# Performance work log

Hardware: AMD Instinct MI355X
Metric: run time of the kernel (lower is better)

The kernel has to match this reference:

```python
import jax, jax.numpy as jnp
import numpy as np

B, NPTS, NBASIS, DIM, H, CH = 8, 1024, 8, 8, 512, 16
EPSILON = 1000.0
P = 2
VOLUME = 2.0 ** DIM  # MC domain [-1,1]^dim


def setup_inputs() -> dict:
    key = jax.random.key(0)
    ks = jax.random.split(key, 10)
    s = jax.random.uniform(ks[0], (NPTS, DIM), dtype=jnp.float32) * 2.0 - 1.0  # MC samples in [-1,1]^dim
    x = jax.random.uniform(ks[1], (1, DIM), dtype=jnp.float32) * 2.0 - 1.0     # eval point
    Wfirst = jax.random.normal(ks[2], (DIM, H), dtype=jnp.float32) / np.sqrt(DIM)
    bfirst = jax.random.normal(ks[3], (H,), dtype=jnp.float32) * 0.01
    Wb = jax.random.normal(ks[4], (NBASIS, H, H), dtype=jnp.float32) / np.sqrt(H)
    bb = jax.random.normal(ks[5], (NBASIS, H), dtype=jnp.float32) * 0.01
    Wlast = jax.random.normal(ks[6], (H, CH), dtype=jnp.float32) / np.sqrt(H)
    blast = jax.random.normal(ks[7], (CH,), dtype=jnp.float32) * 0.01
    Wf = jax.random.normal(ks[8], (DIM, CH), dtype=jnp.float32) / np.sqrt(DIM)
    bf = jax.random.normal(ks[9], (CH,), dtype=jnp.float32) * 0.01
    return dict(s=s, x=x, Wfirst=Wfirst, bfirst=bfirst, Wb=Wb, bb=bb,
                Wlast=Wlast, blast=blast, Wf=Wf, bf=bf)


def _basis_all(pts, Wfirst, bfirst, Wb, bb, Wlast, blast):
    # pts: [M, DIM] -> all n basis nets, batch-repeated: [NBASIS, B, M, CH]
    a0 = jax.nn.elu(jnp.einsum('md,dh->mh', pts, Wfirst) + bfirst)          # [M, H]
    a0 = jnp.broadcast_to(a0[None], (B,) + a0.shape)                         # [B, M, H] (repeat over batch)
    a1 = jax.nn.elu(jnp.einsum('bmh,ihk->ibmk', a0, Wb) + bb[:, None, None, :])  # [n, B, M, H]
    return jnp.einsum('ibmk,kc->ibmc', a1, Wlast) + blast                    # [n, B, M, CH]


def reference(s, x, Wfirst, bfirst, Wb, bb, Wlast, blast, Wf, bf):
    # func(s): linear map realizing the projected function  [NPTS, CH]
    f_s = jnp.einsum('nd,dc->nc', s, Wf) + bf
    basis_s = _basis_all(s, Wfirst, bfirst, Wb, bb, Wlast, blast)            # [n, B, NPTS, CH]
    diff = f_s[None, None] - basis_s                                          # broadcast over n, B
    # Monte Carlo integral of (func - basis_i)^p over [-1,1]^dim, per channel
    integral = VOLUME * jnp.mean(diff ** P, axis=-2)                          # [n, B, CH]
    norm_pc = integral ** (1.0 / P)                                           # Lp norm per channel
    norm_b = jnp.sum(jnp.abs(norm_pc) ** P, axis=-1, keepdims=True) ** (1.0 / P)  # [n, B, 1]
    mu = jnp.where(norm_b <= EPSILON, norm_b, 0.0)                            # [n, B, 1]
    basis_x = _basis_all(x, Wfirst, bfirst, Wb, bb, Wlast, blast)[:, :, 0, :]  # [n, B, CH]
    out = jnp.sum(mu * basis_x, axis=0)                                       # [B, CH]
    normalization = 1e-7 + jnp.sum(mu, axis=0)                                # [B, 1]
    return out / normalization
```

## Files before the change

kernel.cpp:

```cpp
#include <hip/hip_runtime.h>

typedef _Float16 half8 __attribute__((ext_vector_type(8)));
typedef float f32x4 __attribute__((ext_vector_type(4)));
typedef float f32x16 __attribute__((ext_vector_type(16)));
typedef unsigned int u32x4 __attribute__((ext_vector_type(4)));

#define NPTS 1024
#define NB 8
#define HDIM 512
#define CH 16
#define RT 1056

#define OFF_WBH 0u
#define OFF_WBL (4u*1024u*1024u)
#define OFF_A0H (8u*1024u*1024u)
#define A0SZ    (64u*RT*8u*2u)
#define OFF_A0L (OFF_A0H + A0SZ)
#define OFF_WLH (OFF_A0L + A0SZ)
#define OFF_WLL (OFF_WLH + 16384u)
#define OFF_FS  (OFF_WLL + 16384u)
#define OFF_PP  (OFF_FS + 65536u)
#define PPSZ    (8u*2u*RT*16u*4u)
#define OFF_IP  (OFF_PP + PPSZ)
#define OFF_BX  (OFF_IP + 2048u)

__device__ __forceinline__ float elu(float z) { return z > 0.f ? z : expm1f(z); }

__global__ __launch_bounds__(256) void kPrep(const float* __restrict__ s,
    const float* __restrict__ x, const float* __restrict__ Wfirst,
    const float* __restrict__ bfirst, const float* __restrict__ Wb,
    const float* __restrict__ Wlast, const float* __restrict__ Wf,
    const float* __restrict__ bf,
    _Float16* __restrict__ Wbh, _Float16* __restrict__ Wbl,
    _Float16* __restrict__ WlH, _Float16* __restrict__ WlL,
    _Float16* __restrict__ a0h, _Float16* __restrict__ a0l,
    float* __restrict__ f_s) {
  __shared__ __align__(16) float sm[8192];
  int b = blockIdx.x, t = threadIdx.x;
  if (b < 512) {
    int i = b >> 6, koct = b & 63;
    int j = t >> 5, c = t & 31;
    const float* src = Wb + ((size_t)i * 512 + koct * 8 + j) * 512;
#pragma unroll
    for (int e = 0; e < 4; ++e)
      *(f32x4*)&sm[j * 512 + (e * 32 + c) * 4] = *(const f32x4*)&src[(e * 32 + c) * 4];
    __syncthreads();
#pragma unroll
    for (int p = 0; p < 2; ++p) {
      int n = t + p * 256;
      union { _Float16 h[8]; u32x4 u; } hu, lu;
#pragma unroll
      for (int jj = 0; jj < 8; ++jj) {
        float v = sm[jj * 512 + n];
        _Float16 hv = (_Float16)v;
        hu.h[jj] = hv;
        lu.h[jj] = (_Float16)(v - (float)hv);
      }
      size_t o = ((size_t)(i * 64 + koct) * 512 + n) * 8;
      *(u32x4*)(Wbh + o) = hu.u;
      *(u32x4*)(Wbl + o) = lu.u;
    }
  } else if (b < 776) {
    int rr = t >> 6, tl = t & 63;
    int m = (b - 512) * 4 + rr;
    float* sv = &sm[rr * 8];
    if (tl < 8) sv[tl] = (m < 1024) ? s[m * 8 + tl] : (m == 1024 ? x[tl] : 0.f);
    __syncthreads();
    size_t o = ((size_t)tl * RT + m) * 8;
    if (m <= 1024) {
      float acc[8];
#pragma unroll
      for (int jj = 0; jj < 8; ++jj) acc[jj] = bfirst[8 * tl + jj];
#pragma unroll
      for (int d = 0; d < 8; ++d) {
        float sd = sv[d];
        f32x4 w0 = *(const f32x4*)&Wfirst[d * 512 + 8 * tl];
        f32x4 w1 = *(const f32x4*)&Wfirst[d * 512 + 8 * tl + 4];
#pragma unroll
        for (int e = 0; e < 4; ++e) { acc[e] += sd * w0[e]; acc[4 + e] += sd * w1[e]; }
      }
      union { _Float16 h[8]; u32x4 u; } hu, lu;
#pragma unroll
      for (int jj = 0; jj < 8; ++jj) {
        float v = elu(acc[jj]);
        _Float16 hv = (_Float16)v;
        hu.h[jj] = hv;
        lu.h[jj] = (_Float16)(v - (float)hv);
      }
      *(u32x4*)(a0h + o) = hu.u;
      *(u32x4*)(a0l + o) = lu.u;
      if (m < 1024 && tl < 16) {
        float a = bf[tl];
#pragma unroll
        for (int d = 0; d < 8; ++d) a += sv[d] * Wf[d * 16 + tl];
        f_s[m * 16 + tl] = a;
      }
    } else {
      u32x4 z;
#pragma unroll
      for (int e = 0; e < 4; ++e) z[e] = 0u;
      *(u32x4*)(a0h + o) = z;
      *(u32x4*)(a0l + o) = z;
    }
  } else {
#pragma unroll
    for (int it = 0; it < 32; ++it) sm[t + 256 * it] = Wlast[t + 256 * it];
    __syncthreads();
#pragma unroll
    for (int p = 0; p < 4; ++p) {
      int oi = p * 256 + t;
      int ko = oi >> 4, ch = oi & 15;
      union { _Float16 h[8]; u32x4 u; } hu, lu;
#pragma unroll
      for (int jj = 0; jj < 8; ++jj) {
        float v = sm[(ko * 8 + jj) * 16 + ch];
        _Float16 hv = (_Float16)v;
        hu.h[jj] = hv;
        lu.h[jj] = (_Float16)(v - (float)hv);
      }
      *(u32x4*)(WlH + oi * 8) = hu.u;
      *(u32x4*)(WlL + oi * 8) = lu.u;
    }
  }
}

__global__ __launch_bounds__(256, 2) void kB(const _Float16* __restrict__ Wbh,
    const _Float16* __restrict__ Wbl, const _Float16* __restrict__ a0h,
    const _Float16* __restrict__ a0l, const _Float16* __restrict__ WlH,
    const _Float16* __restrict__ WlL, const float* __restrict__ bb,
    float* __restrict__ Pp) {
  __shared__ u32x4 AH[2048];
  __shared__ u32x4 AL[2048];
  __shared__ float S2[32][16];
  int t = threadIdx.x, b = blockIdx.x;
  int i = b & 7, r2 = b >> 3;
  int nh = r2 & 1, mt = r2 >> 1;
  int m0 = mt * 32, nb0 = nh * 256;
  int w = t >> 6, lane = t & 63, ln = lane & 31, q = lane >> 5, q4 = lane >> 4;

  const u32x4* a0h4 = (const u32x4*)a0h;
  const u32x4* a0l4 = (const u32x4*)a0l;
#pragma unroll
  for (int it = 0; it < 8; ++it) {
    int o = t + 256 * it;
    size_t g = (size_t)(o >> 5) * RT + m0 + (o & 31);
    AH[o] = a0h4[g];
    AL[o] = a0l4[g];
  }
  __syncthreads();

  int nwb = nb0 + w * 64;
  const u32x4* bh4 = (const u32x4*)Wbh;
  const u32x4* bl4 = (const u32x4*)Wbl;
  f32x16 hh0, hh1, hl0, hl1, lh0, lh1;
#pragma unroll
  for (int r = 0; r < 16; ++r) { hh0[r]=0.f; hh1[r]=0.f; hl0[r]=0.f; hl1[r]=0.f; lh0[r]=0.f; lh1[r]=0.f; }

#pragma unroll 4
  for (int ks = 0; ks < 32; ++ks) {
    int koct = ks * 2 + q;
    half8 aH = __builtin_bit_cast(half8, AH[koct * 32 + ln]);
    half8 aL = __builtin_bit_cast(half8, AL[koct * 32 + ln]);
    size_t bo = ((size_t)(i * 64 + koct)) * 512 + nwb + ln;
    half8 bH0 = __builtin_bit_cast(half8, bh4[bo]);
    half8 bH1 = __builtin_bit_cast(half8, bh4[bo + 32]);
    half8 bL0 = __builtin_bit_cast(half8, bl4[bo]);
    half8 bL1 = __builtin_bit_cast(half8, bl4[bo + 32]);
    hh0 = __builtin_amdgcn_mfma_f32_32x32x16_f16(aH, bH0, hh0, 0, 0, 0);
    hh1 = __builtin_amdgcn_mfma_f32_32x32x16_f16(aH, bH1, hh1, 0, 0, 0);
    hl0 = __builtin_amdgcn_mfma_f32_32x32x16_f16(aH, bL0, hl0, 0, 0, 0);
    hl1 = __builtin_amdgcn_mfma_f32_32x32x16_f16(aH, bL1, hl1, 0, 0, 0);
    lh0 = __builtin_amdgcn_mfma_f32_32x32x16_f16(aL, bH0, lh0, 0, 0, 0);
    lh1 = __builtin_amdgcn_mfma_f32_32x32x16_f16(aL, bH1, lh1, 0, 0, 0);
  }

  float zv[2][16];
#pragma unroll
  for (int r = 0; r < 16; ++r) {
    zv[0][r] = hh0[r] + hl0[r] + lh0[r];
    zv[1][r] = hh1[r] + hl1[r] + lh1[r];
  }
  __syncthreads();
  for (int o = t; o < 512; o += 256) ((float*)S2)[o] = 0.f;

  _Float16* scrH = (_Float16*)&AH[w * 512];
  _Float16* scrL = (_Float16*)&AH[w * 512 + 256];
#pragma unroll
  for (int nt = 0; nt < 2; ++nt)
#pragma unroll
    for (int r = 0; r < 16; ++r) {
      int row = (r & 3) + 8 * (r >> 2) + 4 * q;
      int kl = nt * 32 + ln;
      int h = nb0 + w * 64 + kl;
      float a1 = elu(zv[nt][r] + bb[i * 512 + h]);
      _Float16 hv = (_Float16)a1;
      _Float16 lv = (_Float16)(a1 - (float)hv);
      int oi = (row >> 4) * 128 + (kl >> 3) * 16 + (row & 15);
      scrH[oi * 8 + (kl & 7)] = hv;
      scrL[oi * 8 + (kl & 7)] = lv;
    }
  __syncthreads();

  int hb8 = (nb0 + w * 64) >> 3;
  const u32x4* wh4 = (const u32x4*)WlH;
  const u32x4* wl4 = (const u32x4*)WlL;
  const u32x4* sH4 = &AH[w * 512];
  const u32x4* sL4 = &AH[w * 512 + 256];
#pragma unroll
  for (int mt2 = 0; mt2 < 2; ++mt2) {
    f32x4 D2;
#pragma unroll
    for (int r = 0; r < 4; ++r) D2[r] = 0.f;
#pragma unroll
    for (int ks2 = 0; ks2 < 2; ++ks2) {
      int ai = mt2 * 128 + (ks2 * 4 + q4) * 16 + (lane & 15);
      half8 pH = __builtin_bit_cast(half8, sH4[ai]);
      half8 pL = __builtin_bit_cast(half8, sL4[ai]);
      size_t wo = (size_t)(hb8 + ks2 * 4 + q4) * 16 + (lane & 15);
      half8 wH = __builtin_bit_cast(half8, wh4[wo]);
      half8 wL = __builtin_bit_cast(half8, wl4[wo]);
      D2 = __builtin_amdgcn_mfma_f32_16x16x32_f16(pH, wH, D2, 0, 0, 0);
      D2 = __builtin_amdgcn_mfma_f32_16x16x32_f16(pH, wL, D2, 0, 0, 0);
      D2 = __builtin_amdgcn_mfma_f32_16x16x32_f16(pL, wH, D2, 0, 0, 0);
    }
#pragma unroll
    for (int r = 0; r < 4; ++r)
      atomicAdd(&S2[mt2 * 16 + q4 * 4 + r][lane & 15], D2[r]);
  }
  __syncthreads();
  for (int o = t; o < 512; o += 256) {
    int m = o >> 4, ch = o & 15;
    Pp[((size_t)(i * 2 + nh) * RT + m0 + m) * 16 + ch] = S2[m][ch];
  }
}

__global__ __launch_bounds__(256) void kTail(const float* __restrict__ Pp,
    const float* __restrict__ f_s, const float* __restrict__ blast,
    float* __restrict__ Ipart, float* __restrict__ basisx) {
  __shared__ float R[16][16];
  int b = blockIdx.x, t = threadIdx.x;
  if (b < 32) {
    int i = b >> 2, mq = b & 3;
    int ch = t & 15, g = t >> 4;
    float bl = blast[ch];
    const float* P0 = Pp + (size_t)(i * 2) * RT * 16;
    const float* P1 = Pp + (size_t)(i * 2 + 1) * RT * 16;
    float loc = 0.f;
#pragma unroll
    for (int it = 0; it < 16; ++it) {
      int m = mq * 256 + g + 16 * it;
      float bs = P0[m * 16 + ch] + P1[m * 16 + ch] + bl;
      float d = f_s[m * 16 + ch] - bs;
      loc += d * d;
    }
    R[g][ch] = loc;
    __syncthreads();
    if (t < 16) {
      float ssum = 0.f;
#pragma unroll
      for (int gg = 0; gg < 16; ++gg) ssum += R[gg][t];
      Ipart[(i * 4 + mq) * 16 + t] = ssum;
    }
  } else if (t < 128) {
    int i = t >> 4, ch = t & 15;
    basisx[t] = Pp[((size_t)(i * 2) * RT + 1024) * 16 + ch]
              + Pp[((size_t)(i * 2 + 1) * RT + 1024) * 16 + ch] + blast[ch];
  }
}

__global__ __launch_bounds__(128) void kFin(const float* __restrict__ Ipart,
    const float* __restrict__ basisx, float* __restrict__ out) {
  __shared__ float muL[8];
  int t = threadIdx.x;
  if (t < 8) {
    float S = 0.f;
#pragma unroll
    for (int qq = 0; qq < 64; ++qq) S += Ipart[t * 64 + qq];
    float nb = 0.5f * sqrtf(S);
    muL[t] = (nb <= 1000.0f) ? nb : 0.f;
  }
  __syncthreads();
  int ch = t & 15;
  float num = 0.f, den = 1e-7f;
#pragma unroll
  for (int i = 0; i < NB; ++i) {
    num += muL[i] * basisx[i * 16 + ch];
    den += muL[i];
  }
  out[t] = num / den;
}

extern "C" void kernel_launch(void* const* d_in, const int* in_sizes, int n_in,
                              void* d_out, int out_size, void* d_ws, size_t ws_size,
                              hipStream_t stream) {
  const float* s      = (const float*)d_in[0];
  const float* x      = (const float*)d_in[1];
  const float* Wfirst = (const float*)d_in[2];
  const float* bfirst = (const float*)d_in[3];
  const float* Wb     = (const float*)d_in[4];
  const float* bb     = (const float*)d_in[5];
  const float* Wlast  = (const float*)d_in[6];
  const float* blast  = (const float*)d_in[7];
  const float* Wf     = (const float*)d_in[8];
  const float* bf     = (const float*)d_in[9];

  char* ws = (char*)d_ws;
  _Float16* Wbh = (_Float16*)(ws + OFF_WBH);
  _Float16* Wbl = (_Float16*)(ws + OFF_WBL);
  _Float16* a0h = (_Float16*)(ws + OFF_A0H);
  _Float16* a0l = (_Float16*)(ws + OFF_A0L);
  _Float16* WlH = (_Float16*)(ws + OFF_WLH);
  _Float16* WlL = (_Float16*)(ws + OFF_WLL);
  float* f_s    = (float*)(ws + OFF_FS);
  float* Pp     = (float*)(ws + OFF_PP);
  float* Ipart  = (float*)(ws + OFF_IP);
  float* basisx = (float*)(ws + OFF_BX);
  float* out    = (float*)d_out;

  kPrep<<<777, 256, 0, stream>>>(s, x, Wfirst, bfirst, Wb, Wlast, Wf, bf,
                                 Wbh, Wbl, WlH, WlL, a0h, a0l, f_s);
  kB<<<528, 256, 0, stream>>>(Wbh, Wbl, a0h, a0l, WlH, WlL, bb, Pp);
  kTail<<<33, 256, 0, stream>>>(Pp, f_s, blast, Ipart, basisx);
  kFin<<<1, 128, 0, stream>>>(Ipart, basisx, out);
}
```

Baseline: 128.6 us.

## Split kB over four N-quarters with register double-buffered global loads

The main GEMM kernel now gives each block a quarter of the hidden dimension (32 columns per wave) instead of half. It drops the LDS staging of a0 and streams A and B fragments straight from global memory into a register double buffer, so the block count doubles and occupancy can rise to three blocks per CU. Weight conversion in kPrep drops its LDS transpose and uses more blocks with strided direct loads. kTail now reduces each basis in a single block and computes mu directly, leaving kFin with less work. The cost is reading a0 from global once per N-quarter with no LDS reuse, and more partial sums in Pp that the tail must read.

```diff
diff --git a/kernel.cpp b/kernel.cpp
--- a/kernel.cpp
+++ b/kernel.cpp
@@ -20,9 +20,9 @@
 #define OFF_WLL (OFF_WLH + 16384u)
 #define OFF_FS  (OFF_WLL + 16384u)
 #define OFF_PP  (OFF_FS + 65536u)
-#define PPSZ    (8u*2u*RT*16u*4u)
-#define OFF_IP  (OFF_PP + PPSZ)
-#define OFF_BX  (OFF_IP + 2048u)
+#define PPSZ    (8u*4u*RT*16u*4u)
+#define OFF_MU  (OFF_PP + PPSZ)
+#define OFF_BX  (OFF_MU + 64u)
 
 __device__ __forceinline__ float elu(float z) { return z > 0.f ? z : expm1f(z); }
 
@@ -37,32 +37,25 @@
     float* __restrict__ f_s) {
   __shared__ __align__(16) float sm[8192];
   int b = blockIdx.x, t = threadIdx.x;
-  if (b < 512) {
-    int i = b >> 6, koct = b & 63;
-    int j = t >> 5, c = t & 31;
-    const float* src = Wb + ((size_t)i * 512 + koct * 8 + j) * 512;
-#pragma unroll
-    for (int e = 0; e < 4; ++e)
-      *(f32x4*)&sm[j * 512 + (e * 32 + c) * 4] = *(const f32x4*)&src[(e * 32 + c) * 4];
-    __syncthreads();
-#pragma unroll
-    for (int p = 0; p < 2; ++p) {
-      int n = t + p * 256;
-      union { _Float16 h[8]; u32x4 u; } hu, lu;
-#pragma unroll
-      for (int jj = 0; jj < 8; ++jj) {
-        float v = sm[jj * 512 + n];
-        _Float16 hv = (_Float16)v;
-        hu.h[jj] = hv;
-        lu.h[jj] = (_Float16)(v - (float)hv);
-      }
-      size_t o = ((size_t)(i * 64 + koct) * 512 + n) * 8;
-      *(u32x4*)(Wbh + o) = hu.u;
-      *(u32x4*)(Wbl + o) = lu.u;
-    }
-  } else if (b < 776) {
+  if (b < 1024) {
+    int i = b >> 7, koct = (b >> 1) & 63, n = (b & 1) * 256 + t;
+    const float* src = Wb + ((size_t)i * 512 + koct * 8) * 512 + n;
+    float v[8];
+#pragma unroll
+    for (int j = 0; j < 8; ++j) v[j] = src[j * 512];
+    union { _Float16 h[8]; u32x4 u; } hu, lu;
+#pragma unroll
+    for (int j = 0; j < 8; ++j) {
+      _Float16 hv = (_Float16)v[j];
+      hu.h[j] = hv;
+      lu.h[j] = (_Float16)(v[j] - (float)hv);
+    }
+    size_t o = ((size_t)(i * 64 + koct) * 512 + n) * 8;
+    *(u32x4*)(Wbh + o) = hu.u;
+    *(u32x4*)(Wbl + o) = lu.u;
+  } else if (b < 1288) {
     int rr = t >> 6, tl = t & 63;
-    int m = (b - 512) * 4 + rr;
+    int m = (b - 1024) * 4 + rr;
     float* sv = &sm[rr * 8];
     if (tl < 8) sv[tl] = (m < 1024) ? s[m * 8 + tl] : (m == 1024 ? x[tl] : 0.f);
     __syncthreads();
@@ -124,161 +117,153 @@
   }
 }
 
-__global__ __launch_bounds__(256, 2) void kB(const _Float16* __restrict__ Wbh,
+__global__ __launch_bounds__(256, 3) void kB(const _Float16* __restrict__ Wbh,
     const _Float16* __restrict__ Wbl, const _Float16* __restrict__ a0h,
     const _Float16* __restrict__ a0l, const _Float16* __restrict__ WlH,
     const _Float16* __restrict__ WlL, const float* __restrict__ bb,
     float* __restrict__ Pp) {
-  __shared__ u32x4 AH[2048];
-  __shared__ u32x4 AL[2048];
+  __shared__ u32x4 SC[1024];
   __shared__ float S2[32][16];
   int t = threadIdx.x, b = blockIdx.x;
-  int i = b & 7, r2 = b >> 3;
-  int nh = r2 & 1, mt = r2 >> 1;
-  int m0 = mt * 32, nb0 = nh * 256;
+  int i = b & 7, r = b >> 3;
+  int nq = r & 3, mt = r >> 2;
+  int m0 = mt * 32;
   int w = t >> 6, lane = t & 63, ln = lane & 31, q = lane >> 5, q4 = lane >> 4;
+  int nw = nq * 128 + w * 32;
 
   const u32x4* a0h4 = (const u32x4*)a0h;
   const u32x4* a0l4 = (const u32x4*)a0l;
-#pragma unroll
-  for (int it = 0; it < 8; ++it) {
-    int o = t + 256 * it;
-    size_t g = (size_t)(o >> 5) * RT + m0 + (o & 31);
-    AH[o] = a0h4[g];
-    AL[o] = a0l4[g];
-  }
-  __syncthreads();
-
-  int nwb = nb0 + w * 64;
-  const u32x4* bh4 = (const u32x4*)Wbh;
-  const u32x4* bl4 = (const u32x4*)Wbl;
-  f32x16 hh0, hh1, hl0, hl1, lh0, lh1;
-#pragma unroll
-  for (int r = 0; r < 16; ++r) { hh0[r]=0.f; hh1[r]=0.f; hl0[r]=0.f; hl1[r]=0.f; lh0[r]=0.f; lh1[r]=0.f; }
-
-#pragma unroll 4
-  for (int ks = 0; ks < 32; ++ks) {
-    int koct = ks * 2 + q;
-    half8 aH = __builtin_bit_cast(half8, AH[koct * 32 + ln]);
-    half8 aL = __builtin_bit_cast(half8, AL[koct * 32 + ln]);
-    size_t bo = ((size_t)(i * 64 + koct)) * 512 + nwb + ln;
-    half8 bH0 = __builtin_bit_cast(half8, bh4[bo]);
-    half8 bH1 = __builtin_bit_cast(half8, bh4[bo + 32]);
-    half8 bL0 = __builtin_bit_cast(half8, bl4[bo]);
-    half8 bL1 = __builtin_bit_cast(half8, bl4[bo + 32]);
-    hh0 = __builtin_amdgcn_mfma_f32_32x32x16_f16(aH, bH0, hh0, 0, 0, 0);
-    hh1 = __builtin_amdgcn_mfma_f32_32x32x16_f16(aH, bH1, hh1, 0, 0, 0);
-    hl0 = __builtin_amdgcn_mfma_f32_32x32x16_f16(aH, bL0, hl0, 0, 0, 0);
-    hl1 = __builtin_amdgcn_mfma_f32_32x32x16_f16(aH, bL1, hl1, 0, 0, 0);
-    lh0 = __builtin_amdgcn_mfma_f32_32x32x16_f16(aL, bH0, lh0, 0, 0, 0);
-    lh1 = __builtin_amdgcn_mfma_f32_32x32x16_f16(aL, bH1, lh1, 0, 0, 0);
-  }
-
-  float zv[2][16];
-#pragma unroll
-  for (int r = 0; r < 16; ++r) {
-    zv[0][r] = hh0[r] + hl0[r] + lh0[r];
-    zv[1][r] = hh1[r] + hl1[r] + lh1[r];
-  }
-  __syncthreads();
-  for (int o = t; o < 512; o += 256) ((float*)S2)[o] = 0.f;
-
-  _Float16* scrH = (_Float16*)&AH[w * 512];
-  _Float16* scrL = (_Float16*)&AH[w * 512 + 256];
-#pragma unroll
-  for (int nt = 0; nt < 2; ++nt)
-#pragma unroll
-    for (int r = 0; r < 16; ++r) {
-      int row = (r & 3) + 8 * (r >> 2) + 4 * q;
-      int kl = nt * 32 + ln;
-      int h = nb0 + w * 64 + kl;
-      float a1 = elu(zv[nt][r] + bb[i * 512 + h]);
-      _Float16 hv = (_Float16)a1;
-      _Float16 lv = (_Float16)(a1 - (float)hv);
-      int oi = (row >> 4) * 128 + (kl >> 3) * 16 + (row & 15);
-      scrH[oi * 8 + (kl & 7)] = hv;
-      scrL[oi * 8 + (kl & 7)] = lv;
-    }
-  __syncthreads();
-
-  int hb8 = (nb0 + w * 64) >> 3;
+  const u32x4* bh4  = (const u32x4*)Wbh;
+  const u32x4* bl4  = (const u32x4*)Wbl;
+  int ma = m0 + ln, nb = nw + ln, ib = i * 64;
+
+  f32x16 hh, hl, lh;
+#pragma unroll
+  for (int rr = 0; rr < 16; ++rr) { hh[rr] = 0.f; hl[rr] = 0.f; lh[rr] = 0.f; }
+
+  u32x4 paH[2][2], paL[2][2], pbH[2][2], pbL[2][2];
+  {
+    int k0 = q, k1 = q + 2;
+    paH[0][0] = a0h4[k0 * RT + ma]; paL[0][0] = a0l4[k0 * RT + ma];
+    paH[0][1] = a0h4[k1 * RT + ma]; paL[0][1] = a0l4[k1 * RT + ma];
+    pbH[0][0] = bh4[(size_t)(ib + k0) * 512 + nb]; pbL[0][0] = bl4[(size_t)(ib + k0) * 512 + nb];
+    pbH[0][1] = bh4[(size_t)(ib + k1) * 512 + nb]; pbL[0][1] = bl4[(size_t)(ib + k1) * 512 + nb];
+  }
+#pragma unroll
+  for (int ks2 = 0; ks2 < 16; ++ks2) {
+    int nx = (ks2 < 15) ? ks2 + 1 : 15;
+    int bn = (ks2 + 1) & 1, bc = ks2 & 1;
+    {
+      int k0 = nx * 4 + q, k1 = k0 + 2;
+      paH[bn][0] = a0h4[k0 * RT + ma]; paL[bn][0] = a0l4[k0 * RT + ma];
+      paH[bn][1] = a0h4[k1 * RT + ma]; paL[bn][1] = a0l4[k1 * RT + ma];
+      pbH[bn][0] = bh4[(size_t)(ib + k0) * 512 + nb]; pbL[bn][0] = bl4[(size_t)(ib + k0) * 512 + nb];
+      pbH[bn][1] = bh4[(size_t)(ib + k1) * 512 + nb]; pbL[bn][1] = bl4[(size_t)(ib + k1) * 512 + nb];
+    }
+#pragma unroll
+    for (int sfx = 0; sfx < 2; ++sfx) {
+      half8 aH = __builtin_bit_cast(half8, paH[bc][sfx]);
+      half8 aL = __builtin_bit_cast(half8, paL[bc][sfx]);
+      half8 bH = __builtin_bit_cast(half8, pbH[bc][sfx]);
+      half8 bL = __builtin_bit_cast(half8, pbL[bc][sfx]);
+      hh = __builtin_amdgcn_mfma_f32_32x32x16_f16(aH, bH, hh, 0, 0, 0);
+      hl = __builtin_amdgcn_mfma_f32_32x32x16_f16(aH, bL, hl, 0, 0, 0);
+      lh = __builtin_amdgcn_mfma_f32_32x32x16_f16(aL, bH, lh, 0, 0, 0);
+    }
+  }
+
+  ((float*)S2)[t] = 0.f;
+  ((float*)S2)[t + 256] = 0.f;
+  float bcol = bb[i * 512 + nw + ln];
+  _Float16* scrH = (_Float16*)&SC[w * 256];
+  _Float16* scrL = (_Float16*)&SC[w * 256 + 128];
+#pragma unroll
+  for (int rr = 0; rr < 16; ++rr) {
+    int row = (rr & 3) + 8 * (rr >> 2) + 4 * q;
+    float a1 = elu(hh[rr] + hl[rr] + lh[rr] + bcol);
+    _Float16 hv = (_Float16)a1;
+    _Float16 lv = (_Float16)(a1 - (float)hv);
+    int oi = (row >> 4) * 64 + (ln >> 3) * 16 + (row & 15);
+    scrH[oi * 8 + (ln & 7)] = hv;
+    scrL[oi * 8 + (ln & 7)] = lv;
+  }
+  __syncthreads();
+
+  const u32x4* sH4 = &SC[w * 256];
+  const u32x4* sL4 = &SC[w * 256 + 128];
   const u32x4* wh4 = (const u32x4*)WlH;
   const u32x4* wl4 = (const u32x4*)WlL;
-  const u32x4* sH4 = &AH[w * 512];
-  const u32x4* sL4 = &AH[w * 512 + 256];
+  int ch = lane & 15;
+  size_t wo = (size_t)((nw >> 3) + q4) * 16 + ch;
+  half8 wH = __builtin_bit_cast(half8, wh4[wo]);
+  half8 wL = __builtin_bit_cast(half8, wl4[wo]);
 #pragma unroll
   for (int mt2 = 0; mt2 < 2; ++mt2) {
     f32x4 D2;
 #pragma unroll
-    for (int r = 0; r < 4; ++r) D2[r] = 0.f;
-#pragma unroll
-    for (int ks2 = 0; ks2 < 2; ++ks2) {
-      int ai = mt2 * 128 + (ks2 * 4 + q4) * 16 + (lane & 15);
-      half8 pH = __builtin_bit_cast(half8, sH4[ai]);
-      half8 pL = __builtin_bit_cast(half8, sL4[ai]);
-      size_t wo = (size_t)(hb8 + ks2 * 4 + q4) * 16 + (lane & 15);
-      half8 wH = __builtin_bit_cast(half8, wh4[wo]);
-      half8 wL = __builtin_bit_cast(half8, wl4[wo]);
-      D2 = __builtin_amdgcn_mfma_f32_16x16x32_f16(pH, wH, D2, 0, 0, 0);
-      D2 = __builtin_amdgcn_mfma_f32_16x16x32_f16(pH, wL, D2, 0, 0, 0);
-      D2 = __builtin_amdgcn_mfma_f32_16x16x32_f16(pL, wH, D2, 0, 0, 0);
-    }
-#pragma unroll
-    for (int r = 0; r < 4; ++r)
-      atomicAdd(&S2[mt2 * 16 + q4 * 4 + r][lane & 15], D2[r]);
+    for (int rr = 0; rr < 4; ++rr) D2[rr] = 0.f;
+    int ai = mt2 * 64 + q4 * 16 + ch;
+    half8 pH = __builtin_bit_cast(half8, sH4[ai]);
+    half8 pL = __builtin_bit_cast(half8, sL4[ai]);
+    D2 = __builtin_amdgcn_mfma_f32_16x16x32_f16(pH, wH, D2, 0, 0, 0);
+    D2 = __builtin_amdgcn_mfma_f32_16x16x32_f16(pH, wL, D2, 0, 0, 0);
+    D2 = __builtin_amdgcn_mfma_f32_16x16x32_f16(pL, wH, D2, 0, 0, 0);
+#pragma unroll
+    for (int rr = 0; rr < 4; ++rr)
+      atomicAdd(&S2[mt2 * 16 + q4 * 4 + rr][ch], D2[rr]);
   }
   __syncthreads();
   for (int o = t; o < 512; o += 256) {
-    int m = o >> 4, ch = o & 15;
-    Pp[((size_t)(i * 2 + nh) * RT + m0 + m) * 16 + ch] = S2[m][ch];
+    int m = o >> 4, c2 = o & 15;
+    Pp[((size_t)(i * 4 + nq) * RT + m0 + m) * 16 + c2] = S2[m][c2];
   }
 }
 
 __global__ __launch_bounds__(256) void kTail(const float* __restrict__ Pp,
     const float* __restrict__ f_s, const float* __restrict__ blast,
-    float* __restrict__ Ipart, float* __restrict__ basisx) {
+    float* __restrict__ mu, float* __restrict__ basisx) {
   __shared__ float R[16][16];
-  int b = blockIdx.x, t = threadIdx.x;
-  if (b < 32) {
-    int i = b >> 2, mq = b & 3;
-    int ch = t & 15, g = t >> 4;
-    float bl = blast[ch];
-    const float* P0 = Pp + (size_t)(i * 2) * RT * 16;
-    const float* P1 = Pp + (size_t)(i * 2 + 1) * RT * 16;
-    float loc = 0.f;
-#pragma unroll
-    for (int it = 0; it < 16; ++it) {
-      int m = mq * 256 + g + 16 * it;
-      float bs = P0[m * 16 + ch] + P1[m * 16 + ch] + bl;
-      float d = f_s[m * 16 + ch] - bs;
-      loc += d * d;
-    }
-    R[g][ch] = loc;
-    __syncthreads();
-    if (t < 16) {
-      float ssum = 0.f;
-#pragma unroll
-      for (int gg = 0; gg < 16; ++gg) ssum += R[gg][t];
-      Ipart[(i * 4 + mq) * 16 + t] = ssum;
-    }
-  } else if (t < 128) {
-    int i = t >> 4, ch = t & 15;
-    basisx[t] = Pp[((size_t)(i * 2) * RT + 1024) * 16 + ch]
-              + Pp[((size_t)(i * 2 + 1) * RT + 1024) * 16 + ch] + blast[ch];
-  }
-}
-
-__global__ __launch_bounds__(128) void kFin(const float* __restrict__ Ipart,
+  __shared__ float sc[16];
+  int i = blockIdx.x, t = threadIdx.x, ch = t & 15, g = t >> 4;
+  const float* P0 = Pp + (size_t)(i * 4) * RT * 16;
+  const size_t PS = (size_t)RT * 16;
+  float bl = blast[ch];
+  float loc = 0.f;
+#pragma unroll 4
+  for (int it = 0; it < 64; ++it) {
+    int m = g + 16 * it;
+    size_t o = (size_t)m * 16 + ch;
+    float bs = P0[o] + P0[PS + o] + P0[2 * PS + o] + P0[3 * PS + o] + bl;
+    float d = f_s[o] - bs;
+    loc += d * d;
+  }
+  R[g][ch] = loc;
+  if (t < 16) {
+    size_t o = (size_t)1024 * 16 + t;
+    basisx[i * 16 + t] = P0[o] + P0[PS + o] + P0[2 * PS + o] + P0[3 * PS + o] + blast[t];
+  }
+  __syncthreads();
+  if (t < 16) {
+    float s2 = 0.f;
+#pragma unroll
+    for (int gg = 0; gg < 16; ++gg) s2 += R[gg][t];
+    sc[t] = s2;
+  }
+  __syncthreads();
+  if (t == 0) {
+    float S = 0.f;
+#pragma unroll
+    for (int c = 0; c < 16; ++c) S += sc[c];
+    float nb = 0.5f * sqrtf(S);
+    mu[i] = (nb <= 1000.0f) ? nb : 0.f;
+  }
+}
+
+__global__ __launch_bounds__(128) void kFin(const float* __restrict__ mu,
     const float* __restrict__ basisx, float* __restrict__ out) {
   __shared__ float muL[8];
   int t = threadIdx.x;
-  if (t < 8) {
-    float S = 0.f;
-#pragma unroll
-    for (int qq = 0; qq < 64; ++qq) S += Ipart[t * 64 + qq];
-    float nb = 0.5f * sqrtf(S);
-    muL[t] = (nb <= 1000.0f) ? nb : 0.f;
-  }
+  if (t < 8) muL[t] = mu[t];
   __syncthreads();
   int ch = t & 15;
   float num = 0.f, den = 1e-7f;
@@ -313,13 +298,13 @@
   _Float16* WlL = (_Float16*)(ws + OFF_WLL);
   float* f_s    = (float*)(ws + OFF_FS);
   float* Pp     = (float*)(ws + OFF_PP);
-  float* Ipart  = (float*)(ws + OFF_IP);
+  float* mu     = (float*)(ws + OFF_MU);
   float* basisx = (float*)(ws + OFF_BX);
   float* out    = (float*)d_out;
 
-  kPrep<<<777, 256, 0, stream>>>(s, x, Wfirst, bfirst, Wb, Wlast, Wf, bf,
-                                 Wbh, Wbl, WlH, WlL, a0h, a0l, f_s);
-  kB<<<528, 256, 0, stream>>>(Wbh, Wbl, a0h, a0l, WlH, WlL, bb, Pp);
-  kTail<<<33, 256, 0, stream>>>(Pp, f_s, blast, Ipart, basisx);
-  kFin<<<1, 128, 0, stream>>>(Ipart, basisx, out);
-}
+  kPrep<<<1289, 256, 0, stream>>>(s, x, Wfirst, bfirst, Wb, Wlast, Wf, bf,
+                                  Wbh, Wbl, WlH, WlL, a0h, a0l, f_s);
+  kB<<<1056, 256, 0, stream>>>(Wbh, Wbl, a0h, a0l, WlH, WlL, bb, Pp);
+  kTail<<<NB, 256, 0, stream>>>(Pp, f_s, blast, mu, basisx);
+  kFin<<<1, 128, 0, stream>>>(mu, basisx, out);
+}
```

New measurement: 139.5 us. +8.5%, slower.
